# Kernel optimization log

Measured on AMD Instinct MI355X. Metric: run time of the kernel, lower is better.

The kernel has to match this reference:

```python
import jax, jax.numpy as jnp
import numpy as np

K, S, PAD = 3, 2, 1
C, HID = 16, 128
H, W = 256, 256
EPS = 1e-6


def _unfold(xp, k, s):
    # xp: (B, C, Hp, Wp) -> (B, C*k*k, L), torch.nn.Unfold ordering (c major, then kh, kw)
    B, Cc, Hp, Wp = xp.shape
    Ho = (Hp - k) // s + 1
    Wo = (Wp - k) // s + 1
    cols = jnp.stack(
        [xp[:, :, i:i + (Ho - 1) * s + 1:s, j:j + (Wo - 1) * s + 1:s]
         for i in range(k) for j in range(k)], axis=2)  # (B, C, k*k, Ho, Wo)
    return cols.reshape(B, Cc * k * k, Ho * Wo), Ho, Wo


def _fold(patches, Hp, Wp, Ho, Wo, k, s):
    # patches: (B, C*k*k, L) -> scatter-add into (B, C, Hp, Wp)
    B = patches.shape[0]
    p = patches.reshape(B, -1, k, k, Ho, Wo)
    out = jnp.zeros((B, p.shape[1], Hp, Wp), dtype=patches.dtype)
    for i in range(k):
        for j in range(k):
            out = out.at[:, :, i:i + (Ho - 1) * s + 1:s, j:j + (Wo - 1) * s + 1:s].add(p[:, :, i, j])
    return out


def setup_inputs() -> dict:
    key = jax.random.key(0)
    ks = jax.random.split(key, 7)
    P = C * K * K  # 144
    x = jax.random.normal(ks[0], (32, C, H, W), dtype=jnp.float32)
    W1 = jax.random.normal(ks[1], (P, HID), dtype=jnp.float32) * (1.0 / np.sqrt(P))
    b1 = jax.random.normal(ks[2], (HID,), dtype=jnp.float32) * 0.01
    W2 = jax.random.normal(ks[3], (HID, P), dtype=jnp.float32) * (1.0 / np.sqrt(HID))
    b2 = jax.random.normal(ks[4], (P,), dtype=jnp.float32) * 0.01
    Wc = jax.random.normal(ks[5], (C, C), dtype=jnp.float32) * (1.0 / np.sqrt(C))
    bc = jax.random.normal(ks[6], (C,), dtype=jnp.float32) * 0.01
    return {"x": x, "W1": W1, "b1": b1, "W2": W2, "b2": b2, "Wc": Wc, "bc": bc}


def reference(x, W1, b1, W2, b2, Wc, bc):
    Hp, Wp = H + 2 * PAD, W + 2 * PAD
    xp = jnp.pad(x, ((0, 0), (0, 0), (PAD, PAD), (PAD, PAD)), mode='reflect')
    patches, Ho, Wo = _unfold(xp, K, S)          # (B, P, L)
    t = patches.transpose(0, 2, 1)               # (B, L, P)
    hcat = jax.nn.relu(t @ W1 + b1)              # (B, L, HID)
    out_p = (hcat @ W2 + b2).transpose(0, 2, 1)  # (B, P, L)
    folded = _fold(out_p, Hp, Wp, Ho, Wo, K, S)
    counts = _fold(jnp.ones_like(out_p), Hp, Wp, Ho, Wo, K, S)
    normalized = folded / (counts + EPS)
    logits = jnp.einsum('oc,bchw->bohw', Wc, normalized) + bc[None, :, None, None]
    attn = jax.nn.softmax(logits, axis=1)        # Softmax2d = softmax over channels
    modulated = normalized * attn
    return modulated[:, :, PAD:PAD + H, PAD:PAD + W]
```

## Files before the change

### kernel.cpp

```cpp
#include <hip/hip_runtime.h>
#include <math.h>

#define CC   16
#define HH   256
#define WW   256
#define HIDN 128
#define PDIM 144
#define K1PAD 160
#define PITCH_H 136
#define PP 2056

typedef _Float16 half8 __attribute__((ext_vector_type(8)));
typedef float   f32x4 __attribute__((ext_vector_type(4)));

#define MFMA16(a, b, c) __builtin_amdgcn_mfma_f32_16x16x32_f16((a), (b), (c), 0, 0, 0)

#define O_BYTES   ((size_t)524288 * 144 * 2)
#define W1T_OFF   O_BYTES
#define W1T_BYTES ((size_t)128 * K1PAD * 2)
#define W2T_OFF   (W1T_OFF + W1T_BYTES)
#define W2T_BYTES ((size_t)144 * 128 * 2)
#define WS_NEEDED (W2T_OFF + W2T_BYTES)

__device__ __forceinline__ void load_lds16(const float* g, float* l)
{
#if __has_builtin(__builtin_amdgcn_global_load_lds)
    __builtin_amdgcn_global_load_lds(
        (const __attribute__((address_space(1))) unsigned int*)g,
        (__attribute__((address_space(3))) unsigned int*)l, 16, 0, 0);
#else
    *(float4*)l = *(const float4*)g;
#endif
}

__device__ __forceinline__ void load_lds16h(const _Float16* g, _Float16* l)
{
#if __has_builtin(__builtin_amdgcn_global_load_lds)
    __builtin_amdgcn_global_load_lds(
        (const __attribute__((address_space(1))) unsigned int*)g,
        (__attribute__((address_space(3))) unsigned int*)l, 16, 0, 0);
#else
    *(float4*)(void*)l = *(const float4*)(const void*)g;
#endif
}

__global__ __launch_bounds__(256) void prep_kernel(
    const float* __restrict__ W1, const float* __restrict__ W2,
    _Float16* __restrict__ W1T, _Float16* __restrict__ W2T)
{
    const int idx = blockIdx.x * 256 + threadIdx.x;
    if (idx < 128 * K1PAD) {
        const int n = idx / K1PAD;
        const int k = idx - n * K1PAD;
        const int tap = k >> 4;
        const int c   = k & 15;
        W1T[idx] = (tap < 9) ? (_Float16)W1[(c * 9 + tap) * HIDN + n] : (_Float16)0.f;
    }
    if (idx < 144 * 128) {
        const int nn = idx >> 7;
        const int k  = idx & 127;
        const int tap = nn >> 4;
        const int c   = nn & 15;
        W2T[nn * 128 + k] = (_Float16)W2[k * PDIM + (c * 9 + tap)];
    }
}

__global__ __launch_bounds__(512) void mlp_kernel(
    const float* __restrict__ x,
    const _Float16* __restrict__ W1T, const float* __restrict__ b1,
    const _Float16* __restrict__ W2T, const float* __restrict__ b2,
    _Float16* __restrict__ og)
{
    __shared__ __align__(16) char smem[73728];
    _Float16* xT    = (_Float16*)smem;
    float*    xrowF = (float*)(smem + 24576);
    _Float16* hT    = (_Float16*)(smem + 24576);

    const int tid   = threadIdx.x;
    const int a     = blockIdx.x & 127;
    const int batch = blockIdx.x >> 7;
    const float* xb = x + (size_t)batch * CC * HH * WW;

    #pragma unroll
    for (int it = 0; it < 6; ++it) {
        const int idx = tid + it * 512;
        const int i   = idx >> 10;
        const int c   = (idx >> 6) & 15;
        const int q   = idx & 63;
        int ym = 2 * a + i - 1;
        if (ym < 0) ym = 1;
        load_lds16(xb + ((c * HH + ym) * WW + 4 * q), xrowF + idx * 4);
    }
    __syncthreads();

    #pragma unroll
    for (int k = 0; k < 2; ++k) {
        const int u = tid + k * 512;
        if (u < 768) {
            const int i  = u >> 8;
            const int xm = u & 255;
            const float* rbase = xrowF + i * 4096 + xm;
            half8 lo, hi;
            #pragma unroll
            for (int c = 0; c < 8; ++c) lo[c] = (_Float16)rbase[c * 256];
            #pragma unroll
            for (int c = 0; c < 8; ++c) hi[c] = (_Float16)rbase[(c + 8) * 256];
            int s = u << 4;
            s ^= (s & 0x1C0) >> 3;
            *(half8*)(xT + s)       = lo;
            *(half8*)(xT + (s ^ 8)) = hi;
        }
    }
    __syncthreads();

    const int wid  = tid >> 6;
    const int lane = tid & 63;
    const int l15  = lane & 15;
    const int quad = lane >> 4;
    const int qh   = quad >> 1;
    const int c0   = (quad & 1) * 8;
    const int wm   = wid >> 2;
    const int wn   = wid & 3;

    {
        half8 bfr0[5], bfr1[5];
        float bias0, bias1;
        {
            const int nt0 = 2 * wn, nt1 = 2 * wn + 1;
            const _Float16* w0 = W1T + (nt0 * 16 + l15) * K1PAD + quad * 8;
            const _Float16* w1 = W1T + (nt1 * 16 + l15) * K1PAD + quad * 8;
            #pragma unroll
            for (int ks = 0; ks < 5; ++ks) {
                bfr0[ks] = *(const half8*)(w0 + ks * 32);
                bfr1[ks] = *(const half8*)(w1 + ks * 32);
            }
            bias0 = b1[nt0 * 16 + l15];
            bias1 = b1[nt1 * 16 + l15];
        }
        int koffU[5], koffF[5];
        #pragma unroll
        for (int ks = 0; ks < 5; ++ks) {
            int tap = 2 * ks + qh;
            if (tap > 8) tap = 8;
            const int i   = (tap * 11) >> 5;
            const int j   = tap - 3 * i;
            const int xmU = 2 * l15 + j - 1;
            const int xmF = (xmU < 0) ? 1 : xmU;
            koffU[ks] = (i << 12) + (xmU << 4) + c0;
            koffF[ks] = (i << 12) + (xmF << 4) + c0;
        }

        #define G1_STEP(MT, KO)                                                   \
        {                                                                         \
            f32x4 acc0 = {0.f, 0.f, 0.f, 0.f};                                    \
            f32x4 acc1 = {0.f, 0.f, 0.f, 0.f};                                    \
            _Pragma("unroll")                                                     \
            for (int ks = 0; ks < 5; ++ks) {                                      \
                int ix = KO[ks] + ((MT) << 9);                                    \
                ix ^= (ix & 0x1C0) >> 3;                                          \
                const half8 af = *(const half8*)(xT + ix);                        \
                acc0 = MFMA16(af, bfr0[ks], acc0);                                \
                acc1 = MFMA16(af, bfr1[ks], acc1);                                \
            }                                                                     \
            _Pragma("unroll")                                                     \
            for (int r = 0; r < 4; ++r) {                                         \
                const int row = (MT) * 16 + quad * 4 + r;                         \
                float h0 = acc0[r] + bias0;                                       \
                float h1 = acc1[r] + bias1;                                       \
                hT[row * PITCH_H + (2 * wn) * 16 + l15]     = (_Float16)(h0 > 0.f ? h0 : 0.f); \
                hT[row * PITCH_H + (2 * wn + 1) * 16 + l15] = (_Float16)(h1 > 0.f ? h1 : 0.f); \
            }                                                                     \
        }

        if (wm == 0) {
            G1_STEP(0, koffF)
            #pragma unroll
            for (int mt = 1; mt < 4; ++mt) G1_STEP(mt, koffU)
        } else {
            #pragma unroll
            for (int mt = 4; mt < 8; ++mt) G1_STEP(mt, koffU)
        }
        #undef G1_STEP
    }
    __syncthreads();

    const size_t abase = ((size_t)batch * 128 + a) * 9;
    {
        half8 bfr2[2][4];
        float bias2[2];
        #pragma unroll
        for (int n = 0; n < 2; ++n) {
            const int nt = 2 * wn + n;
            const _Float16* w2row = W2T + (nt * 16 + l15) * 128 + quad * 8;
            #pragma unroll
            for (int ks = 0; ks < 4; ++ks)
                bfr2[n][ks] = *(const half8*)(w2row + ks * 32);
            bias2[n] = b2[l15 * 9 + nt];
        }
        _Float16* ognA = og + (abase + 2 * wn) * 2048;
        _Float16* ognB = og + (abase + 2 * wn + 1) * 2048;
        #pragma unroll
        for (int m = 0; m < 4; ++m) {
            const int mt = wm * 4 + m;
            f32x4 acc0 = {0.f, 0.f, 0.f, 0.f};
            f32x4 acc1 = {0.f, 0.f, 0.f, 0.f};
            const _Float16* arow = hT + (mt * 16 + l15) * PITCH_H + quad * 8;
            #pragma unroll
            for (int ks = 0; ks < 4; ++ks) {
                const half8 af = *(const half8*)(arow + ks * 32);
                acc0 = MFMA16(af, bfr2[0][ks], acc0);
                acc1 = MFMA16(af, bfr2[1][ks], acc1);
            }
            #pragma unroll
            for (int r = 0; r < 4; ++r) {
                const int b = mt * 16 + quad * 4 + r;
                ognA[b * 16 + l15] = (_Float16)(acc0[r] + bias2[0]);
                ognB[b * 16 + l15] = (_Float16)(acc1[r] + bias2[1]);
            }
        }
        {
            half8 bfr8[4];
            const _Float16* w2row = W2T + (8 * 16 + l15) * 128 + quad * 8;
            #pragma unroll
            for (int ks = 0; ks < 4; ++ks)
                bfr8[ks] = *(const half8*)(w2row + ks * 32);
            const float bias8 = b2[l15 * 9 + 8];
            _Float16* ogn = og + (abase + 8) * 2048;
            const int mt = wid;
            f32x4 acc = {0.f, 0.f, 0.f, 0.f};
            const _Float16* arow = hT + (mt * 16 + l15) * PITCH_H + quad * 8;
            #pragma unroll
            for (int ks = 0; ks < 4; ++ks)
                acc = MFMA16(*(const half8*)(arow + ks * 32), bfr8[ks], acc);
            #pragma unroll
            for (int r = 0; r < 4; ++r) {
                const int b = mt * 16 + quad * 4 + r;
                ogn[b * 16 + l15] = (_Float16)(acc[r] + bias8);
            }
        }
    }
}

__global__ __launch_bounds__(256) void gather_kernel(
    const _Float16* __restrict__ og, const float* __restrict__ Wc,
    const float* __restrict__ bc, float* __restrict__ out)
{
    __shared__ __align__(16) _Float16 sPl[6 * PP];
    __shared__ float sWc[256];
    __shared__ float sbc[16];

    const int tid   = threadIdx.x;
    const int y     = blockIdx.x & 255;
    const int batch = blockIdx.x >> 8;

    sWc[tid] = Wc[tid];
    if (tid < 16) sbc[tid] = bc[tid];

    int alist[2], ilist[2], na = 0;
    if ((y + 1) & 1) { alist[0] = y >> 1; ilist[0] = 1; na = 1; }
    else {
        if (y < 255) { alist[na] = (y + 1) >> 1; ilist[na] = 0; ++na; }
        alist[na] = (y - 1) >> 1; ilist[na] = 2; ++na;
    }

    const size_t pb = (size_t)batch * 128;
    for (int p = 0; p < na * 3; ++p) {
        const int u   = (p >= 3) ? 1 : 0;
        const int j   = p - 3 * u;
        const int tap = ilist[u] * 3 + j;
        const _Float16* src = og + ((pb + alist[u]) * 9 + tap) * 2048 + tid * 8;
        load_lds16h(src, sPl + p * PP + tid * 8);
    }
    __syncthreads();

    const int x = tid;
    int blist[2], jlist[2], nb = 0;
    if ((x + 1) & 1) { blist[0] = x >> 1; jlist[0] = 1; nb = 1; }
    else {
        if (x < 255) { blist[nb] = (x + 1) >> 1; jlist[nb] = 0; ++nb; }
        blist[nb] = (x - 1) >> 1; jlist[nb] = 2; ++nb;
    }

    float nrm[CC];
    #pragma unroll
    for (int c = 0; c < CC; ++c) nrm[c] = 0.f;

    for (int u = 0; u < 2; ++u) {
        if (u >= na) break;
        for (int v = 0; v < 2; ++v) {
            if (v >= nb) break;
            const _Float16* orow = sPl + (u * 3 + jlist[v]) * PP + blist[v] * 16;
            const half8 o0 = *(const half8*)(orow);
            const half8 o1 = *(const half8*)(orow + 8);
            #pragma unroll
            for (int e = 0; e < 8; ++e) { nrm[e] += (float)o0[e]; nrm[8 + e] += (float)o1[e]; }
        }
    }
    const float inv = 1.f / ((float)(na * nb) + 1e-6f);
    #pragma unroll
    for (int c = 0; c < CC; ++c) nrm[c] *= inv;

    float lg[CC];
    #pragma unroll
    for (int o = 0; o < CC; ++o) {
        float s = sbc[o];
        #pragma unroll
        for (int c = 0; c < CC; ++c) s = fmaf(sWc[o * CC + c], nrm[c], s);
        lg[o] = s;
    }
    float mx = lg[0];
    #pragma unroll
    for (int o = 1; o < CC; ++o) mx = fmaxf(mx, lg[o]);
    float se = 0.f;
    #pragma unroll
    for (int o = 0; o < CC; ++o) { lg[o] = expf(lg[o] - mx); se += lg[o]; }
    const float isum = 1.f / se;

    const size_t obase = ((size_t)batch * CC) * (HH * WW) + (size_t)y * WW + x;
    #pragma unroll
    for (int c = 0; c < CC; ++c)
        out[obase + (size_t)c * (HH * WW)] = nrm[c] * lg[c] * isum;
}

#define HT_PITCH 68
__global__ __launch_bounds__(256) void mlp_fold_kernel_fb(
    const float* __restrict__ x,  const float* __restrict__ W1,
    const float* __restrict__ b1, const float* __restrict__ W2,
    const float* __restrict__ b2, float* __restrict__ folded)
{
    __shared__ __align__(16) float pT[PDIM * 64];
    __shared__ __align__(16) float hT[HIDN * HT_PITCH];
    const int tid = threadIdx.x;
    const int tile = blockIdx.x & 255;
    const int b = blockIdx.x >> 8;
    const int tile_base = tile * 64;
    const float* xb = x + (size_t)b * CC * HH * WW;
    for (int idx = tid; idx < PDIM * 64; idx += 256) {
        const int p = idx >> 6, lo = idx & 63;
        const int c = p / 9, rem = p - c * 9, i = rem / 3, j = rem - i * 3;
        const int l = tile_base + lo, a = l >> 7, bb = l & 127;
        int ym = 2 * a + i - 1, xm = 2 * bb + j - 1;
        if (ym < 0) ym = 1;
        if (xm < 0) xm = 1;
        pT[p * 64 + lo] = xb[(c * HH + ym) * WW + xm];
    }
    __syncthreads();
    {
        const int cg = tid & 31, rg = tid >> 5, rbase = rg * 8;
        float acc[8][4];
        #pragma unroll
        for (int m = 0; m < 8; ++m)
            #pragma unroll
            for (int jj = 0; jj < 4; ++jj) acc[m][jj] = 0.f;
        for (int k = 0; k < PDIM; ++k) {
            const float4 w = *reinterpret_cast<const float4*>(W1 + k * HIDN + cg * 4);
            const float4 pa = *reinterpret_cast<const float4*>(pT + k * 64 + rbase);
            const float4 pb2 = *reinterpret_cast<const float4*>(pT + k * 64 + rbase + 4);
            const float pv[8] = {pa.x, pa.y, pa.z, pa.w, pb2.x, pb2.y, pb2.z, pb2.w};
            const float wv[4] = {w.x, w.y, w.z, w.w};
            #pragma unroll
            for (int m = 0; m < 8; ++m)
                #pragma unroll
                for (int jj = 0; jj < 4; ++jj) acc[m][jj] = fmaf(pv[m], wv[jj], acc[m][jj]);
        }
        #pragma unroll
        for (int jj = 0; jj < 4; ++jj) {
            const int jcol = cg * 4 + jj;
            const float bj = b1[jcol];
            #pragma unroll
            for (int m = 0; m < 8; ++m) {
                const float hval = acc[m][jj] + bj;
                hT[jcol * HT_PITCH + rbase + m] = hval > 0.f ? hval : 0.f;
            }
        }
    }
    __syncthreads();
    {
        const int cg2 = tid & 15, rg2 = tid >> 4, rb2 = rg2 * 4;
        float acc2[4][9];
        #pragma unroll
        for (int m = 0; m < 4; ++m)
            #pragma unroll
            for (int jj = 0; jj < 9; ++jj) acc2[m][jj] = 0.f;
        const float* w2base = W2 + cg2 * 9;
        for (int h = 0; h < HIDN; ++h) {
            const float4 hv4 = *reinterpret_cast<const float4*>(hT + h * HT_PITCH + rb2);
            const float hv[4] = {hv4.x, hv4.y, hv4.z, hv4.w};
            float wv[9];
            #pragma unroll
            for (int jj = 0; jj < 9; ++jj) wv[jj] = w2base[h * PDIM + jj];
            #pragma unroll
            for (int m = 0; m < 4; ++m)
                #pragma unroll
                for (int jj = 0; jj < 9; ++jj) acc2[m][jj] = fmaf(hv[m], wv[jj], acc2[m][jj]);
        }
        float bv[9];
        #pragma unroll
        for (int jj = 0; jj < 9; ++jj) bv[jj] = b2[cg2 * 9 + jj];
        float* fb = folded + ((size_t)b * CC + cg2) * (HH * WW);
        #pragma unroll
        for (int m = 0; m < 4; ++m) {
            const int l = tile_base + rb2 + m, a = l >> 7, bb = l & 127;
            #pragma unroll
            for (int jj = 0; jj < 9; ++jj) {
                const int i = jj / 3, j2 = jj - i * 3;
                const int ypad = 2 * a + i, xpad = 2 * bb + j2;
                if (ypad >= 1 && xpad >= 1)
                    atomicAdd(fb + (ypad - 1) * WW + (xpad - 1), acc2[m][jj] + bv[jj]);
            }
        }
    }
}

__global__ __launch_bounds__(256) void norm_softmax_kernel_fb(
    float* __restrict__ out, const float* __restrict__ Wc, const float* __restrict__ bc)
{
    const int xo = threadIdx.x, yo = blockIdx.x & 255, b = blockIdx.x >> 8;
    const int yp = yo + 1, xp = xo + 1;
    const float cy = ((yp & 1) || yp == 256) ? 1.f : 2.f;
    const float cx = ((xp & 1) || xp == 256) ? 1.f : 2.f;
    const float inv = 1.f / (cy * cx + 1e-6f);
    const size_t base = ((size_t)b * CC) * (HH * WW) + (size_t)yo * WW + xo;
    float nrm[CC];
    #pragma unroll
    for (int c = 0; c < CC; ++c) nrm[c] = out[base + (size_t)c * (HH * WW)] * inv;
    float logits[CC];
    #pragma unroll
    for (int o = 0; o < CC; ++o) {
        float s = bc[o];
        #pragma unroll
        for (int c = 0; c < CC; ++c) s = fmaf(Wc[o * CC + c], nrm[c], s);
        logits[o] = s;
    }
    float mx = logits[0];
    #pragma unroll
    for (int o = 1; o < CC; ++o) mx = fmaxf(mx, logits[o]);
    float se = 0.f;
    #pragma unroll
    for (int o = 0; o < CC; ++o) { logits[o] = expf(logits[o] - mx); se += logits[o]; }
    const float isum = 1.f / se;
    #pragma unroll
    for (int c = 0; c < CC; ++c)
        out[base + (size_t)c * (HH * WW)] = nrm[c] * logits[c] * isum;
}

extern "C" void kernel_launch(void* const* d_in, const int* in_sizes, int n_in,
                              void* d_out, int out_size, void* d_ws, size_t ws_size,
                              hipStream_t stream)
{
    const float* x  = (const float*)d_in[0];
    const float* W1 = (const float*)d_in[1];
    const float* b1 = (const float*)d_in[2];
    const float* W2 = (const float*)d_in[3];
    const float* b2 = (const float*)d_in[4];
    const float* Wc = (const float*)d_in[5];
    const float* bc = (const float*)d_in[6];
    float* out = (float*)d_out;

    if (ws_size >= WS_NEEDED) {
        _Float16* og  = (_Float16*)d_ws;
        _Float16* W1T = (_Float16*)((char*)d_ws + W1T_OFF);
        _Float16* W2T = (_Float16*)((char*)d_ws + W2T_OFF);

        prep_kernel<<<dim3(80), dim3(256), 0, stream>>>(W1, W2, W1T, W2T);
        mlp_kernel<<<dim3(32 * 128), dim3(512), 0, stream>>>(x, W1T, b1, W2T, b2, og);
        gather_kernel<<<dim3(32 * 256), dim3(256), 0, stream>>>(og, Wc, bc, out);
    } else {
        hipMemsetAsync(d_out, 0, (size_t)out_size * sizeof(float), stream);
        mlp_fold_kernel_fb<<<dim3(32 * 256), dim3(256), 0, stream>>>(x, W1, b1, W2, b2, out);
        norm_softmax_kernel_fb<<<dim3(32 * 256), dim3(256), 0, stream>>>(out, Wc, bc);
    }
}
```

Measured before the change: 349.5 us.

## Gather two output rows per block and halve MLP block size

The gather kernel now handles a pair of output rows (2a, 2a+1) per block. It loads nine tap planes once, from patch rows a and a+1, and shares the middle plane set between both rows, which cuts redundant og reads and halves the grid. LDS reads use an XOR swizzle that matches the layout of the load source. The MLP kernel drops from 512 to 256 threads, so each wave covers all eight M tiles for two N tiles. This trades per-block parallelism for more blocks per CU and more register reuse of weight fragments.

After: 332.2 us. 1.05x faster.

```diff
diff --git a/kernel.cpp b/kernel.cpp
--- a/kernel.cpp
+++ b/kernel.cpp
@@ -8,7 +8,6 @@
 #define PDIM 144
 #define K1PAD 160
 #define PITCH_H 136
-#define PP 2056
 
 typedef _Float16 half8 __attribute__((ext_vector_type(8)));
 typedef float   f32x4 __attribute__((ext_vector_type(4)));
@@ -65,7 +64,7 @@
     }
 }
 
-__global__ __launch_bounds__(512) void mlp_kernel(
+__global__ __launch_bounds__(256) void mlp_kernel(
     const float* __restrict__ x,
     const _Float16* __restrict__ W1T, const float* __restrict__ b1,
     const _Float16* __restrict__ W2T, const float* __restrict__ b2,
@@ -82,8 +81,8 @@
     const float* xb = x + (size_t)batch * CC * HH * WW;
 
     #pragma unroll
-    for (int it = 0; it < 6; ++it) {
-        const int idx = tid + it * 512;
+    for (int it = 0; it < 12; ++it) {
+        const int idx = tid + it * 256;
         const int i   = idx >> 10;
         const int c   = (idx >> 6) & 15;
         const int q   = idx & 63;
@@ -94,22 +93,20 @@
     __syncthreads();
 
     #pragma unroll
-    for (int k = 0; k < 2; ++k) {
-        const int u = tid + k * 512;
-        if (u < 768) {
-            const int i  = u >> 8;
-            const int xm = u & 255;
-            const float* rbase = xrowF + i * 4096 + xm;
-            half8 lo, hi;
-            #pragma unroll
-            for (int c = 0; c < 8; ++c) lo[c] = (_Float16)rbase[c * 256];
-            #pragma unroll
-            for (int c = 0; c < 8; ++c) hi[c] = (_Float16)rbase[(c + 8) * 256];
-            int s = u << 4;
-            s ^= (s & 0x1C0) >> 3;
-            *(half8*)(xT + s)       = lo;
-            *(half8*)(xT + (s ^ 8)) = hi;
-        }
+    for (int k = 0; k < 3; ++k) {
+        const int u  = tid + k * 256;
+        const int i  = u >> 8;
+        const int xm = u & 255;
+        const float* rbase = xrowF + i * 4096 + xm;
+        half8 lo, hi;
+        #pragma unroll
+        for (int c = 0; c < 8; ++c) lo[c] = (_Float16)rbase[c * 256];
+        #pragma unroll
+        for (int c = 0; c < 8; ++c) hi[c] = (_Float16)rbase[(c + 8) * 256];
+        int s = u << 4;
+        s ^= (s & 0x1C0) >> 3;
+        *(half8*)(xT + s)       = lo;
+        *(half8*)(xT + (s ^ 8)) = hi;
     }
     __syncthreads();
 
@@ -119,14 +116,12 @@
     const int quad = lane >> 4;
     const int qh   = quad >> 1;
     const int c0   = (quad & 1) * 8;
-    const int wm   = wid >> 2;
-    const int wn   = wid & 3;
 
     {
         half8 bfr0[5], bfr1[5];
         float bias0, bias1;
         {
-            const int nt0 = 2 * wn, nt1 = 2 * wn + 1;
+            const int nt0 = 2 * wid, nt1 = 2 * wid + 1;
             const _Float16* w0 = W1T + (nt0 * 16 + l15) * K1PAD + quad * 8;
             const _Float16* w1 = W1T + (nt1 * 16 + l15) * K1PAD + quad * 8;
             #pragma unroll
@@ -167,19 +162,13 @@
                 const int row = (MT) * 16 + quad * 4 + r;                         \
                 float h0 = acc0[r] + bias0;                                       \
                 float h1 = acc1[r] + bias1;                                       \
-                hT[row * PITCH_H + (2 * wn) * 16 + l15]     = (_Float16)(h0 > 0.f ? h0 : 0.f); \
-                hT[row * PITCH_H + (2 * wn + 1) * 16 + l15] = (_Float16)(h1 > 0.f ? h1 : 0.f); \
+                hT[row * PITCH_H + (2 * wid) * 16 + l15]     = (_Float16)(h0 > 0.f ? h0 : 0.f); \
+                hT[row * PITCH_H + (2 * wid + 1) * 16 + l15] = (_Float16)(h1 > 0.f ? h1 : 0.f); \
             }                                                                     \
         }
 
-        if (wm == 0) {
-            G1_STEP(0, koffF)
-            #pragma unroll
-            for (int mt = 1; mt < 4; ++mt) G1_STEP(mt, koffU)
-        } else {
-            #pragma unroll
-            for (int mt = 4; mt < 8; ++mt) G1_STEP(mt, koffU)
-        }
+        G1_STEP(0, koffF)
+        for (int mt = 1; mt < 8; ++mt) G1_STEP(mt, koffU)
         #undef G1_STEP
     }
     __syncthreads();
@@ -190,18 +179,16 @@
         float bias2[2];
         #pragma unroll
         for (int n = 0; n < 2; ++n) {
-            const int nt = 2 * wn + n;
+            const int nt = wid + n * 4;
             const _Float16* w2row = W2T + (nt * 16 + l15) * 128 + quad * 8;
             #pragma unroll
             for (int ks = 0; ks < 4; ++ks)
                 bfr2[n][ks] = *(const half8*)(w2row + ks * 32);
             bias2[n] = b2[l15 * 9 + nt];
         }
-        _Float16* ognA = og + (abase + 2 * wn) * 2048;
-        _Float16* ognB = og + (abase + 2 * wn + 1) * 2048;
-        #pragma unroll
-        for (int m = 0; m < 4; ++m) {
-            const int mt = wm * 4 + m;
+        _Float16* ognA = og + (abase + wid) * 2048;
+        _Float16* ognB = og + (abase + wid + 4) * 2048;
+        for (int mt = 0; mt < 8; ++mt) {
             f32x4 acc0 = {0.f, 0.f, 0.f, 0.f};
             f32x4 acc1 = {0.f, 0.f, 0.f, 0.f};
             const _Float16* arow = hT + (mt * 16 + l15) * PITCH_H + quad * 8;
@@ -226,16 +213,19 @@
                 bfr8[ks] = *(const half8*)(w2row + ks * 32);
             const float bias8 = b2[l15 * 9 + 8];
             _Float16* ogn = og + (abase + 8) * 2048;
-            const int mt = wid;
-            f32x4 acc = {0.f, 0.f, 0.f, 0.f};
-            const _Float16* arow = hT + (mt * 16 + l15) * PITCH_H + quad * 8;
-            #pragma unroll
-            for (int ks = 0; ks < 4; ++ks)
-                acc = MFMA16(*(const half8*)(arow + ks * 32), bfr8[ks], acc);
-            #pragma unroll
-            for (int r = 0; r < 4; ++r) {
-                const int b = mt * 16 + quad * 4 + r;
-                ogn[b * 16 + l15] = (_Float16)(acc[r] + bias8);
+            #pragma unroll
+            for (int m = 0; m < 2; ++m) {
+                const int mt = 2 * wid + m;
+                f32x4 acc = {0.f, 0.f, 0.f, 0.f};
+                const _Float16* arow = hT + (mt * 16 + l15) * PITCH_H + quad * 8;
+                #pragma unroll
+                for (int ks = 0; ks < 4; ++ks)
+                    acc = MFMA16(*(const half8*)(arow + ks * 32), bfr8[ks], acc);
+                #pragma unroll
+                for (int r = 0; r < 4; ++r) {
+                    const int b = mt * 16 + quad * 4 + r;
+                    ogn[b * 16 + l15] = (_Float16)(acc[r] + bias8);
+                }
             }
         }
     }
@@ -245,31 +235,26 @@
     const _Float16* __restrict__ og, const float* __restrict__ Wc,
     const float* __restrict__ bc, float* __restrict__ out)
 {
-    __shared__ __align__(16) _Float16 sPl[6 * PP];
+    __shared__ __align__(16) _Float16 sPl[9 * 2048];
     __shared__ float sWc[256];
     __shared__ float sbc[16];
 
     const int tid   = threadIdx.x;
-    const int y     = blockIdx.x & 255;
-    const int batch = blockIdx.x >> 8;
+    const int a     = blockIdx.x & 127;
+    const int batch = blockIdx.x >> 7;
 
     sWc[tid] = Wc[tid];
     if (tid < 16) sbc[tid] = bc[tid];
 
-    int alist[2], ilist[2], na = 0;
-    if ((y + 1) & 1) { alist[0] = y >> 1; ilist[0] = 1; na = 1; }
-    else {
-        if (y < 255) { alist[na] = (y + 1) >> 1; ilist[na] = 0; ++na; }
-        alist[na] = (y - 1) >> 1; ilist[na] = 2; ++na;
-    }
-
     const size_t pb = (size_t)batch * 128;
-    for (int p = 0; p < na * 3; ++p) {
-        const int u   = (p >= 3) ? 1 : 0;
-        const int j   = p - 3 * u;
-        const int tap = ilist[u] * 3 + j;
-        const _Float16* src = og + ((pb + alist[u]) * 9 + tap) * 2048 + tid * 8;
-        load_lds16h(src, sPl + p * PP + tid * 8);
+    const int a1 = (a < 127) ? a + 1 : 127;
+    const int srcOff = (tid ^ ((tid >> 3) & 7)) * 8;
+    #pragma unroll
+    for (int p = 0; p < 9; ++p) {
+        const int ap  = (p < 6) ? a : a1;
+        const int tap = (p < 3) ? (3 + p) : ((p < 6) ? (3 + p) : (p - 6));
+        const _Float16* src = og + ((pb + ap) * 9 + tap) * 2048 + srcOff;
+        load_lds16h(src, sPl + p * 2048 + tid * 8);
     }
     __syncthreads();
 
@@ -280,46 +265,62 @@
         if (x < 255) { blist[nb] = (x + 1) >> 1; jlist[nb] = 0; ++nb; }
         blist[nb] = (x - 1) >> 1; jlist[nb] = 2; ++nb;
     }
-
-    float nrm[CC];
-    #pragma unroll
-    for (int c = 0; c < CC; ++c) nrm[c] = 0.f;
-
-    for (int u = 0; u < 2; ++u) {
-        if (u >= na) break;
-        for (int v = 0; v < 2; ++v) {
-            if (v >= nb) break;
-            const _Float16* orow = sPl + (u * 3 + jlist[v]) * PP + blist[v] * 16;
-            const half8 o0 = *(const half8*)(orow);
-            const half8 o1 = *(const half8*)(orow + 8);
-            #pragma unroll
-            for (int e = 0; e < 8; ++e) { nrm[e] += (float)o0[e]; nrm[8 + e] += (float)o1[e]; }
-        }
-    }
-    const float inv = 1.f / ((float)(na * nb) + 1e-6f);
-    #pragma unroll
-    for (int c = 0; c < CC; ++c) nrm[c] *= inv;
-
-    float lg[CC];
-    #pragma unroll
-    for (int o = 0; o < CC; ++o) {
-        float s = sbc[o];
-        #pragma unroll
-        for (int c = 0; c < CC; ++c) s = fmaf(sWc[o * CC + c], nrm[c], s);
-        lg[o] = s;
-    }
-    float mx = lg[0];
-    #pragma unroll
-    for (int o = 1; o < CC; ++o) mx = fmaxf(mx, lg[o]);
-    float se = 0.f;
-    #pragma unroll
-    for (int o = 0; o < CC; ++o) { lg[o] = expf(lg[o] - mx); se += lg[o]; }
-    const float isum = 1.f / se;
-
-    const size_t obase = ((size_t)batch * CC) * (HH * WW) + (size_t)y * WW + x;
-    #pragma unroll
-    for (int c = 0; c < CC; ++c)
-        out[obase + (size_t)c * (HH * WW)] = nrm[c] * lg[c] * isum;
+    const int na1 = (a < 127) ? 2 : 1;
+
+    float nrm0[CC], nrm1[CC];
+    #pragma unroll
+    for (int c = 0; c < CC; ++c) { nrm0[c] = 0.f; nrm1[c] = 0.f; }
+
+    #define ACC_PLANE(P, B, DST)                                             \
+    {                                                                        \
+        int s = (B) * 16;                                                    \
+        s ^= (s & 0x1C0) >> 3;                                               \
+        const _Float16* orow = sPl + (P) * 2048;                             \
+        const half8 o0 = *(const half8*)(orow + s);                          \
+        const half8 o1 = *(const half8*)(orow + (s ^ 8));                    \
+        _Pragma("unroll")                                                    \
+        for (int e = 0; e < 8; ++e) { DST[e] += (float)o0[e]; DST[8 + e] += (float)o1[e]; } \
+    }
+
+    for (int v = 0; v < 2; ++v) {
+        if (v >= nb) break;
+        const int j = jlist[v];
+        const int b = blist[v];
+        ACC_PLANE(j,     b, nrm0)
+        ACC_PLANE(3 + j, b, nrm1)
+        if (na1 == 2) ACC_PLANE(6 + j, b, nrm1)
+    }
+    #undef ACC_PLANE
+
+    const float inv0 = 1.f / ((float)nb + 1e-6f);
+    const float inv1 = 1.f / ((float)(na1 * nb) + 1e-6f);
+    #pragma unroll
+    for (int c = 0; c < CC; ++c) { nrm0[c] *= inv0; nrm1[c] *= inv1; }
+
+    const size_t obase = ((size_t)batch * CC) * (HH * WW) + (size_t)(2 * a) * WW + x;
+    #pragma unroll
+    for (int rowsel = 0; rowsel < 2; ++rowsel) {
+        const float* nrm = rowsel ? nrm1 : nrm0;
+        float lg[CC];
+        #pragma unroll
+        for (int o = 0; o < CC; ++o) {
+            float s = sbc[o];
+            #pragma unroll
+            for (int c = 0; c < CC; ++c) s = fmaf(sWc[o * CC + c], nrm[c], s);
+            lg[o] = s;
+        }
+        float mx = lg[0];
+        #pragma unroll
+        for (int o = 1; o < CC; ++o) mx = fmaxf(mx, lg[o]);
+        float se = 0.f;
+        #pragma unroll
+        for (int o = 0; o < CC; ++o) { lg[o] = expf(lg[o] - mx); se += lg[o]; }
+        const float isum = 1.f / se;
+        const size_t ob = obase + (size_t)rowsel * WW;
+        #pragma unroll
+        for (int c = 0; c < CC; ++c)
+            out[ob + (size_t)c * (HH * WW)] = nrm[c] * lg[c] * isum;
+    }
 }
 
 #define HT_PITCH 68
@@ -463,8 +464,8 @@
         _Float16* W2T = (_Float16*)((char*)d_ws + W2T_OFF);
 
         prep_kernel<<<dim3(80), dim3(256), 0, stream>>>(W1, W2, W1T, W2T);
-        mlp_kernel<<<dim3(32 * 128), dim3(512), 0, stream>>>(x, W1T, b1, W2T, b2, og);
-        gather_kernel<<<dim3(32 * 256), dim3(256), 0, stream>>>(og, Wc, bc, out);
+        mlp_kernel<<<dim3(32 * 128), dim3(256), 0, stream>>>(x, W1T, b1, W2T, b2, og);
+        gather_kernel<<<dim3(32 * 128), dim3(256), 0, stream>>>(og, Wc, bc, out);
     } else {
         hipMemsetAsync(d_out, 0, (size_t)out_size * sizeof(float), stream);
         mlp_fold_kernel_fb<<<dim3(32 * 256), dim3(256), 0, stream>>>(x, W1, b1, W2, b2, out);
```
